# Performance work log

Measured on AMD Instinct MI355X. Metric: run time of the kernel, lower is better.

The kernel has to match this reference:

```python
import jax, jax.numpy as jnp
import numpy as np

SEQ_LEN, BATCH, HIDDEN, NUM_LAYERS = 512, 64, 1024, 2

def setup_inputs() -> dict:
    key = jax.random.key(0)
    k_x, k_w, k_b = jax.random.split(key, 3)
    std = 1.0 / np.sqrt(HIDDEN)
    x = jax.random.normal(k_x, (SEQ_LEN, BATCH, HIDDEN), dtype=jnp.float32)
    # per-layer cell params: W [2H, 4H], b [4H], uniform(-std, std) as in reset_parameters
    W = jax.random.uniform(k_w, (NUM_LAYERS, 2 * HIDDEN, 4 * HIDDEN), minval=-std, maxval=std, dtype=jnp.float32)
    b = jax.random.uniform(k_b, (NUM_LAYERS, 4 * HIDDEN), minval=-std, maxval=std, dtype=jnp.float32)
    return {"x": x, "W": W, "b": b}

def _cell(x_t, h_prev, c_prev, W, b):
    # gates = [x_t, h_prev] @ W + b ; chunk order: f, i, g, o
    gates = jnp.concatenate([x_t, h_prev], axis=1) @ W + b  # [B, 4H]
    f, i, g, o = jnp.split(gates, 4, axis=1)
    f = jax.nn.sigmoid(f)
    i = jax.nn.sigmoid(i)
    g = jnp.tanh(g)
    o = jax.nn.sigmoid(o)
    c_t = f * c_prev + i * g
    h_t = o * jnp.tanh(c_t)
    return h_t, c_t

def reference(x, W, b):
    T, B, _ = x.shape
    L, _, fourH = W.shape
    H = fourH // 4
    h0 = jnp.zeros((L, B, H), dtype=x.dtype)
    c0 = jnp.zeros((L, B, H), dtype=x.dtype)

    def step(carry, x_t):
        h, c = carry  # each [L, B, H]
        new_h, new_c = [], []
        inp = x_t
        for l in range(L):  # small fixed layer count
            h_l, c_l = _cell(inp, h[l], c[l], W[l], b[l])
            new_h.append(h_l)
            new_c.append(c_l)
            inp = h_l
        return (jnp.stack(new_h), jnp.stack(new_c)), inp

    (h_n, c_n), output = jax.lax.scan(step, (h0, c0), x)
    return output, (h_n, c_n)
```

## Files before the change

### kernel.cpp

```cpp
#include <hip/hip_runtime.h>
#include <math.h>


#define T_STEPS 512
#define HID     1024
#define STATE   65536
#define G4      4096

typedef _Float16 f16;
typedef _Float16 f16x8 __attribute__((ext_vector_type(8)));
typedef float    f32x4 __attribute__((ext_vector_type(4)));

__device__ __forceinline__ float sigf(float x) { return 1.0f / (1.0f + __expf(-x)); }

__global__ __launch_bounds__(256) void pack_w(const float* __restrict__ W,
                                              f16* __restrict__ packW)
{
    const size_t g = (size_t)blockIdx.x * 256 + threadIdx.x;
    const int lane = g & 63;
    const int ksg  = (g >> 6) & 63;
    const int nt   = (g >> 12) & 255;
    const int l    = (int)(g >> 20);
    const int k    = ksg * 32 + ((lane >> 4) << 3);
    const int n    = nt * 16 + (lane & 15);
    const float* src = W + ((size_t)l * 2048 + k) * G4 + n;
    f16x8 v;
    #pragma unroll
    for (int j = 0; j < 8; ++j) v[j] = (f16)src[(size_t)j * G4];
    *(f16x8*)(packW + g * 8) = v;
}

__global__ __launch_bounds__(256) void cvt_x0(const float* __restrict__ x,
                                              f16* __restrict__ xf)
{
    const int i = blockIdx.x * 256 + threadIdx.x;
    xf[i] = (f16)x[i];
}

__global__ __launch_bounds__(512) void step_kernel(
    const f16* __restrict__ packW, const float* __restrict__ bias,
    const float* __restrict__ x,
    f16* __restrict__ xf16_0, f16* __restrict__ xf16_1,
    f16* __restrict__ h0_0, f16* __restrict__ h0_1,
    f16* __restrict__ h1_0, f16* __restrict__ h1_1,
    float* __restrict__ h0f32,
    float* __restrict__ c0, float* __restrict__ c1,
    float* __restrict__ out, int d)
{
    const int layer = blockIdx.x >> 7;
    const int mhalf = (blockIdx.x >> 6) & 1;
    const int strip = blockIdx.x & 63;
    const int act   = layer ? (d >= 1) : (d < T_STEPS);
    const int tid   = threadIdx.x;

    __shared__ float red[8][32][68];

    const f16* xf_cur  = (d & 1) ? xf16_1 : xf16_0;
    const f16* h0_prev = ((d + 1) & 1) ? h0_1 : h0_0;
    const f16* h1_prev = ((d + 1) & 1) ? h1_1 : h1_0;
    f16* h0_new = (d & 1) ? h0_1 : h0_0;
    f16* h1_new = (d & 1) ? h1_1 : h1_0;

    if (act) {
        const int w = tid >> 6, lane = tid & 63;
        const f16* Abase = (layer == 0) ? ((w < 4) ? xf_cur : h0_prev)
                                        : ((w < 4) ? h0_prev : h1_prev);
        const int kloc = (w & 3) * 256;
        const int am = lane & 15, ak = (lane >> 4) * 8;
        const int abrow = mhalf * 32 + am;

        f32x4 acc[2][4];
        #pragma unroll
        for (int mt = 0; mt < 2; ++mt)
            #pragma unroll
            for (int g = 0; g < 4; ++g) acc[mt][g] = (f32x4){0.f, 0.f, 0.f, 0.f};

        const size_t fb = ((size_t)layer * 256 + strip) * 64 + w * 8;

        for (int ks = 0; ks < 8; ++ks) {
            const int kk = kloc + ks * 32 + ak;
            f16x8 a[2], b[4];
            #pragma unroll
            for (int mt = 0; mt < 2; ++mt)
                a[mt] = *(const f16x8*)(Abase + (size_t)(abrow + mt * 16) * HID + kk);
            #pragma unroll
            for (int g = 0; g < 4; ++g)
                b[g] = *(const f16x8*)(packW + (fb + (size_t)g * 64 * 64 + ks) * 512
                                       + lane * 8);
            #pragma unroll
            for (int mt = 0; mt < 2; ++mt)
                #pragma unroll
                for (int g = 0; g < 4; ++g)
                    acc[mt][g] = __builtin_amdgcn_mfma_f32_16x16x32_f16(
                        a[mt], b[g], acc[mt][g], 0, 0, 0);
        }
        const int rbase = (lane >> 4) * 4;
        const int cn    = lane & 15;
        #pragma unroll
        for (int mt = 0; mt < 2; ++mt)
            #pragma unroll
            for (int g = 0; g < 4; ++g)
                #pragma unroll
                for (int r = 0; r < 4; ++r)
                    red[w][mt * 16 + rbase + r][g * 16 + cn] = acc[mt][g][r];
    }
    __syncthreads();

    if (act) {
        const int jq   = tid & 15;
        const int mrow = tid >> 4;
        const int b    = mhalf * 32 + mrow;
        const int jgl  = strip * 16 + jq;

        float gate[4];
        #pragma unroll
        for (int g = 0; g < 4; ++g) {
            float s = bias[layer * G4 + g * HID + jgl];
            #pragma unroll
            for (int w = 0; w < 8; ++w) s += red[w][mrow][g * 16 + jq];
            gate[g] = s;
        }
        const float f  = sigf(gate[0]);
        const float i  = sigf(gate[1]);
        const float gg = tanhf(gate[2]);
        const float o  = sigf(gate[3]);

        const int e = b * HID + jgl;
        float* c = layer ? c1 : c0;
        const float cn = f * c[e] + i * gg;
        c[e] = cn;
        const float hn = o * tanhf(cn);
        if (layer) { h1_new[e] = (f16)hn; out[(size_t)(d - 1) * STATE + e] = hn; }
        else       { h0_new[e] = (f16)hn; h0f32[e] = hn; }
    }

    if (d + 1 < T_STEPS) {
        const int idx = blockIdx.x * 512 + tid;
        if (idx < STATE) {
            f16* xdst = ((d + 1) & 1) ? xf16_1 : xf16_0;
            xdst[idx] = (f16)x[(size_t)(d + 1) * STATE + idx];
        }
    }
}

__global__ __launch_bounds__(256) void finalize(
    const float* __restrict__ h0f32, const float* __restrict__ c0,
    const float* __restrict__ c1, float* __restrict__ out)
{
    const int i = blockIdx.x * 256 + threadIdx.x;
    float* dst = out + (size_t)T_STEPS * STATE;
    dst[i]             = h0f32[i];
    dst[STATE + i]     = out[(size_t)(T_STEPS - 1) * STATE + i];
    dst[2 * STATE + i] = c0[i];
    dst[3 * STATE + i] = c1[i];
}

extern "C" void kernel_launch(void* const* d_in, const int* in_sizes, int n_in,
                              void* d_out, int out_size, void* d_ws, size_t ws_size,
                              hipStream_t stream)
{
    const float* x    = (const float*)d_in[0];
    const float* W    = (const float*)d_in[1];
    const float* bias = (const float*)d_in[2];
    float* out = (float*)d_out;

    f16* packW  = (f16*)d_ws;
    f16* xf16_0 = packW + (size_t)2 * 256 * 64 * 512;
    f16* xf16_1 = xf16_0 + STATE;
    f16* h0_0   = xf16_1 + STATE;
    f16* h0_1   = h0_0 + STATE;
    f16* h1_0   = h0_1 + STATE;
    f16* h1_1   = h1_0 + STATE;
    float* h0f32 = (float*)(h1_1 + STATE);
    float* c0    = h0f32 + STATE;
    float* c1    = c0 + STATE;

    hipMemsetAsync(h0_0, 0, (size_t)4 * STATE * 2 + (size_t)3 * STATE * 4, stream);
    pack_w<<<8192, 256, 0, stream>>>(W, packW);
    cvt_x0<<<STATE / 256, 256, 0, stream>>>(x, xf16_0);

    for (int d = 0; d <= T_STEPS; ++d) {
        step_kernel<<<256, 512, 0, stream>>>(packW, bias, x,
                                             xf16_0, xf16_1,
                                             h0_0, h0_1, h1_0, h1_1,
                                             h0f32, c0, c1, out, d);
    }
    finalize<<<STATE / 256, 256, 0, stream>>>(h0f32, c0, c1, out);
}
```

Before: 6.463 ms.

## Replace per-step launches with persistent LSTM kernel using grid barrier and register-resident weights

Replaces the 513 per-timestep kernel launches with one persistent kernel of 256 workgroups that loop over time and synchronize through an atomic grid barrier. Each workgroup keeps its weight slice in registers for the whole run, and the cell state lives in a register instead of global memory. Weights are repacked so each workgroup owns 8 hidden columns across all four gates and all 64 batch rows. The intent is to remove launch overhead and the repeated weight and state reloads. In exchange it depends on all 256 workgroups being co-resident and adds spin-wait barrier cost and register pressure.

```diff
diff --git a/kernel.cpp b/kernel.cpp
--- a/kernel.cpp
+++ b/kernel.cpp
@@ -6,6 +6,8 @@
 #define HID     1024
 #define STATE   65536
 #define G4      4096
+#define NWG     256
+#define NCG     128
 
 typedef _Float16 f16;
 typedef _Float16 f16x8 __attribute__((ext_vector_type(8)));
@@ -14,20 +16,25 @@
 __device__ __forceinline__ float sigf(float x) { return 1.0f / (1.0f + __expf(-x)); }
 
 __global__ __launch_bounds__(256) void pack_w(const float* __restrict__ W,
-                                              f16* __restrict__ packW)
+                                              f16* __restrict__ pw)
 {
-    const size_t g = (size_t)blockIdx.x * 256 + threadIdx.x;
-    const int lane = g & 63;
-    const int ksg  = (g >> 6) & 63;
-    const int nt   = (g >> 12) & 255;
-    const int l    = (int)(g >> 20);
-    const int k    = ksg * 32 + ((lane >> 4) << 3);
-    const int n    = nt * 16 + (lane & 15);
+    const size_t gt = (size_t)blockIdx.x * 256 + threadIdx.x;
+    const int lane = gt & 63;
+    const size_t f = gt >> 6;
+    const int nf = (int)(f & 1);
+    const int ks = (int)((f >> 1) & 63);
+    const int cg = (int)((f >> 7) & (NCG - 1));
+    const int l  = (int)(f >> 14);
+    const int s  = lane & 15;
+    const int g  = nf * 2 + (s >> 3);
+    const int c  = s & 7;
+    const int k  = ks * 32 + ((lane >> 4) << 3);
+    const int n  = g * HID + cg * 8 + c;
     const float* src = W + ((size_t)l * 2048 + k) * G4 + n;
     f16x8 v;
     #pragma unroll
     for (int j = 0; j < 8; ++j) v[j] = (f16)src[(size_t)j * G4];
-    *(f16x8*)(packW + g * 8) = v;
+    *(f16x8*)(pw + gt * 8) = v;
 }
 
 __global__ __launch_bounds__(256) void cvt_x0(const float* __restrict__ x,
@@ -37,122 +44,132 @@
     xf[i] = (f16)x[i];
 }
 
-__global__ __launch_bounds__(512) void step_kernel(
-    const f16* __restrict__ packW, const float* __restrict__ bias,
-    const float* __restrict__ x,
-    f16* __restrict__ xf16_0, f16* __restrict__ xf16_1,
-    f16* __restrict__ h0_0, f16* __restrict__ h0_1,
-    f16* __restrict__ h1_0, f16* __restrict__ h1_1,
-    float* __restrict__ h0f32,
-    float* __restrict__ c0, float* __restrict__ c1,
-    float* __restrict__ out, int d)
+__device__ __forceinline__ void gbar(unsigned* bar, unsigned target)
 {
-    const int layer = blockIdx.x >> 7;
-    const int mhalf = (blockIdx.x >> 6) & 1;
-    const int strip = blockIdx.x & 63;
-    const int act   = layer ? (d >= 1) : (d < T_STEPS);
-    const int tid   = threadIdx.x;
-
-    __shared__ float red[8][32][68];
-
-    const f16* xf_cur  = (d & 1) ? xf16_1 : xf16_0;
-    const f16* h0_prev = ((d + 1) & 1) ? h0_1 : h0_0;
-    const f16* h1_prev = ((d + 1) & 1) ? h1_1 : h1_0;
-    f16* h0_new = (d & 1) ? h0_1 : h0_0;
-    f16* h1_new = (d & 1) ? h1_1 : h1_0;
-
-    if (act) {
-        const int w = tid >> 6, lane = tid & 63;
-        const f16* Abase = (layer == 0) ? ((w < 4) ? xf_cur : h0_prev)
-                                        : ((w < 4) ? h0_prev : h1_prev);
-        const int kloc = (w & 3) * 256;
-        const int am = lane & 15, ak = (lane >> 4) * 8;
-        const int abrow = mhalf * 32 + am;
-
-        f32x4 acc[2][4];
-        #pragma unroll
-        for (int mt = 0; mt < 2; ++mt)
-            #pragma unroll
-            for (int g = 0; g < 4; ++g) acc[mt][g] = (f32x4){0.f, 0.f, 0.f, 0.f};
-
-        const size_t fb = ((size_t)layer * 256 + strip) * 64 + w * 8;
-
-        for (int ks = 0; ks < 8; ++ks) {
-            const int kk = kloc + ks * 32 + ak;
-            f16x8 a[2], b[4];
-            #pragma unroll
-            for (int mt = 0; mt < 2; ++mt)
-                a[mt] = *(const f16x8*)(Abase + (size_t)(abrow + mt * 16) * HID + kk);
-            #pragma unroll
-            for (int g = 0; g < 4; ++g)
-                b[g] = *(const f16x8*)(packW + (fb + (size_t)g * 64 * 64 + ks) * 512
-                                       + lane * 8);
-            #pragma unroll
-            for (int mt = 0; mt < 2; ++mt)
-                #pragma unroll
-                for (int g = 0; g < 4; ++g)
-                    acc[mt][g] = __builtin_amdgcn_mfma_f32_16x16x32_f16(
-                        a[mt], b[g], acc[mt][g], 0, 0, 0);
-        }
-        const int rbase = (lane >> 4) * 4;
-        const int cn    = lane & 15;
-        #pragma unroll
-        for (int mt = 0; mt < 2; ++mt)
-            #pragma unroll
-            for (int g = 0; g < 4; ++g)
-                #pragma unroll
-                for (int r = 0; r < 4; ++r)
-                    red[w][mt * 16 + rbase + r][g * 16 + cn] = acc[mt][g][r];
+    __syncthreads();
+    if (threadIdx.x == 0) {
+        __threadfence();
+        __hip_atomic_fetch_add(bar, 1u, __ATOMIC_RELAXED, __HIP_MEMORY_SCOPE_AGENT);
+        while (__hip_atomic_load(bar, __ATOMIC_RELAXED, __HIP_MEMORY_SCOPE_AGENT) < target)
+            __builtin_amdgcn_s_sleep(4);
+        __threadfence();
     }
     __syncthreads();
+}
 
-    if (act) {
-        const int jq   = tid & 15;
-        const int mrow = tid >> 4;
-        const int b    = mhalf * 32 + mrow;
-        const int jgl  = strip * 16 + jq;
+__global__ __launch_bounds__(512, 2) void lstm_persist(
+    const f16* __restrict__ pw, const float* __restrict__ bias,
+    const float* __restrict__ x,
+    f16* xf0, f16* xf1,
+    f16* h0a, f16* h0b, f16* h1a, f16* h1b,
+    unsigned* bar, float* out)
+{
+    const int wgid  = blockIdx.x;
+    const int layer = wgid >> 7;
+    const int cg    = wgid & (NCG - 1);
+    const int tid   = threadIdx.x;
+    const int w     = tid >> 6;
+    const int lane  = tid & 63;
 
-        float gate[4];
+    __shared__ __align__(16) float red[8][32][68];
+
+    f16x8 wf[8][2];
+    {
+        const f16* base = pw + ((((size_t)layer * NCG + cg) * 64 + w * 8) * 2) * 512
+                             + lane * 8;
         #pragma unroll
-        for (int g = 0; g < 4; ++g) {
-            float s = bias[layer * G4 + g * HID + jgl];
+        for (int q = 0; q < 8; ++q)
             #pragma unroll
-            for (int w = 0; w < 8; ++w) s += red[w][mrow][g * 16 + jq];
-            gate[g] = s;
-        }
-        const float f  = sigf(gate[0]);
-        const float i  = sigf(gate[1]);
-        const float gg = tanhf(gate[2]);
-        const float o  = sigf(gate[3]);
-
-        const int e = b * HID + jgl;
-        float* c = layer ? c1 : c0;
-        const float cn = f * c[e] + i * gg;
-        c[e] = cn;
-        const float hn = o * tanhf(cn);
-        if (layer) { h1_new[e] = (f16)hn; out[(size_t)(d - 1) * STATE + e] = hn; }
-        else       { h0_new[e] = (f16)hn; h0f32[e] = hn; }
+            for (int nf = 0; nf < 2; ++nf)
+                wf[q][nf] = *(const f16x8*)(base + (q * 2 + nf) * 512);
     }
 
-    if (d + 1 < T_STEPS) {
-        const int idx = blockIdx.x * 512 + tid;
-        if (idx < STATE) {
-            f16* xdst = ((d + 1) & 1) ? xf16_1 : xf16_0;
-            xdst[idx] = (f16)x[(size_t)(d + 1) * STATE + idx];
+    const int crow = tid >> 3;
+    const int ccol = tid & 7;
+    float bgate[4];
+    #pragma unroll
+    for (int g = 0; g < 4; ++g) bgate[g] = bias[layer * G4 + g * HID + cg * 8 + ccol];
+    float creg = 0.0f;
+
+    const int am    = lane & 15;
+    const int ak    = (lane >> 4) << 3;
+    const int kbase = (w & 3) * 256;
+
+    float* dst = out + (size_t)T_STEPS * STATE;
+
+    for (int d = 0; d <= T_STEPS; ++d) {
+        const int act = layer ? (d >= 1) : (d < T_STEPS);
+        const f16* xf_cur  = (d & 1) ? xf1 : xf0;
+        const f16* h0_prev = (d & 1) ? h0a : h0b;
+        const f16* h1_prev = (d & 1) ? h1a : h1b;
+        f16* h0_new = (d & 1) ? h0b : h0a;
+        f16* h1_new = (d & 1) ? h1b : h1a;
+
+        if (act) {
+            const f16* Ab = (layer == 0) ? ((w < 4) ? xf_cur  : h0_prev)
+                                         : ((w < 4) ? h0_prev : h1_prev);
+            f32x4 acc[4][2] = {};
+            #pragma unroll
+            for (int q = 0; q < 8; ++q) {
+                const int kk = kbase + q * 32 + ak;
+                f16x8 a[4];
+                #pragma unroll
+                for (int m = 0; m < 4; ++m)
+                    a[m] = *(const f16x8*)(Ab + (size_t)(m * 16 + am) * HID + kk);
+                #pragma unroll
+                for (int m = 0; m < 4; ++m) {
+                    acc[m][0] = __builtin_amdgcn_mfma_f32_16x16x32_f16(
+                        a[m], wf[q][0], acc[m][0], 0, 0, 0);
+                    acc[m][1] = __builtin_amdgcn_mfma_f32_16x16x32_f16(
+                        a[m], wf[q][1], acc[m][1], 0, 0, 0);
+                }
+            }
+            const int srow = (lane >> 4) * 4;
+            const int slot = lane & 15;
+            #pragma unroll
+            for (int m = 0; m < 4; ++m) {
+                *(f32x4*)&red[w][slot]     [m * 16 + srow] = acc[m][0];
+                *(f32x4*)&red[w][16 + slot][m * 16 + srow] = acc[m][1];
+            }
         }
+        __syncthreads();
+
+        if (act) {
+            float gate[4];
+            #pragma unroll
+            for (int g = 0; g < 4; ++g) {
+                float s = bgate[g];
+                #pragma unroll
+                for (int wv = 0; wv < 8; ++wv) s += red[wv][g * 8 + ccol][crow];
+                gate[g] = s;
+            }
+            const float fg = sigf(gate[0]);
+            const float ig = sigf(gate[1]);
+            const float gg = tanhf(gate[2]);
+            const float og = sigf(gate[3]);
+            creg = fg * creg + ig * gg;
+            const float hn = og * tanhf(creg);
+            const int e = crow * HID + cg * 8 + ccol;
+            if (layer) {
+                h1_new[e] = (f16)hn;
+                out[(size_t)(d - 1) * STATE + e] = hn;
+                if (d == T_STEPS) dst[STATE + e] = hn;
+            } else {
+                h0_new[e] = (f16)hn;
+                if (d == T_STEPS - 1) dst[e] = hn;
+            }
+        }
+
+        if (d + 1 < T_STEPS && tid < 256) {
+            const int idx = wgid * 256 + tid;
+            f16* xd = ((d + 1) & 1) ? xf1 : xf0;
+            xd[idx] = (f16)x[(size_t)(d + 1) * STATE + idx];
+        }
+
+        if (d < T_STEPS) gbar(bar, (unsigned)(d + 1) * NWG);
     }
-}
 
-__global__ __launch_bounds__(256) void finalize(
-    const float* __restrict__ h0f32, const float* __restrict__ c0,
-    const float* __restrict__ c1, float* __restrict__ out)
-{
-    const int i = blockIdx.x * 256 + threadIdx.x;
-    float* dst = out + (size_t)T_STEPS * STATE;
-    dst[i]             = h0f32[i];
-    dst[STATE + i]     = out[(size_t)(T_STEPS - 1) * STATE + i];
-    dst[2 * STATE + i] = c0[i];
-    dst[3 * STATE + i] = c1[i];
+    dst[2 * STATE + (size_t)layer * STATE + crow * HID + cg * 8 + ccol] = creg;
 }
 
 extern "C" void kernel_launch(void* const* d_in, const int* in_sizes, int n_in,
@@ -164,26 +181,19 @@
     const float* bias = (const float*)d_in[2];
     float* out = (float*)d_out;
 
-    f16* packW  = (f16*)d_ws;
-    f16* xf16_0 = packW + (size_t)2 * 256 * 64 * 512;
-    f16* xf16_1 = xf16_0 + STATE;
-    f16* h0_0   = xf16_1 + STATE;
-    f16* h0_1   = h0_0 + STATE;
-    f16* h1_0   = h0_1 + STATE;
-    f16* h1_1   = h1_0 + STATE;
-    float* h0f32 = (float*)(h1_1 + STATE);
-    float* c0    = h0f32 + STATE;
-    float* c1    = c0 + STATE;
+    f16* pw  = (f16*)d_ws;
+    f16* xf0 = pw + (size_t)2 * NCG * 64 * 2 * 512;
+    f16* xf1 = xf0 + STATE;
+    f16* h0a = xf1 + STATE;
+    f16* h0b = h0a + STATE;
+    f16* h1a = h0b + STATE;
+    f16* h1b = h1a + STATE;
+    unsigned* bar = (unsigned*)(h1b + STATE);
 
-    hipMemsetAsync(h0_0, 0, (size_t)4 * STATE * 2 + (size_t)3 * STATE * 4, stream);
-    pack_w<<<8192, 256, 0, stream>>>(W, packW);
-    cvt_x0<<<STATE / 256, 256, 0, stream>>>(x, xf16_0);
+    hipMemsetAsync(xf0, 0, (size_t)6 * STATE * sizeof(f16) + 256, stream);
+    pack_w<<<8192, 256, 0, stream>>>(W, pw);
+    cvt_x0<<<STATE / 256, 256, 0, stream>>>(x, xf0);
 
-    for (int d = 0; d <= T_STEPS; ++d) {
-        step_kernel<<<256, 512, 0, stream>>>(packW, bias, x,
-                                             xf16_0, xf16_1,
-                                             h0_0, h0_1, h1_0, h1_1,
-                                             h0f32, c0, c1, out, d);
-    }
-    finalize<<<STATE / 256, 256, 0, stream>>>(h0f32, c0, c1, out);
+    lstm_persist<<<NWG, 512, 0, stream>>>(pw, bias, x, xf0, xf1,
+                                          h0a, h0b, h1a, h1b, bar, out);
 }
```

New measurement: 14.55 ms. +125.1%, slower.
